# Kernel tuning notes

Measured on AMD Instinct MI355X. Metric: run time of the kernel, lower is better.

The kernel has to match this reference:

```python
import jax, jax.numpy as jnp
import numpy as np

D_MODEL = 1024
N_HEAD = 16
D_HEAD = D_MODEL // N_HEAD
B, S = 4, 2048


def setup_inputs() -> dict:
    key = jax.random.key(0)
    ks = jax.random.split(key, 9)
    s = 1.0 / np.sqrt(D_MODEL)
    inp = {"x": jax.random.normal(ks[0], (B, S, D_MODEL), dtype=jnp.float32)}
    for i, name in enumerate(["q", "k", "v", "o"]):
        inp[f"W{name}"] = jax.random.uniform(ks[1 + 2 * i], (D_MODEL, D_MODEL), jnp.float32, -s, s)
        inp[f"b{name}"] = jax.random.uniform(ks[2 + 2 * i], (D_MODEL,), jnp.float32, -s, s)
    return inp


def reference(x, Wq, bq, Wk, bk, Wv, bv, Wo, bo):
    b, sq, _ = x.shape
    skv = sq
    # projections (torch Linear: x @ W^T + b), reshape to (b, h, s, d)
    def proj(W, bias):
        return (x @ W.T + bias).reshape(b, sq, N_HEAD, D_HEAD).transpose(0, 2, 1, 3)
    q, k, v = proj(Wq, bq), proj(Wk, bk), proj(Wv, bv)
    scale = np.sqrt(D_HEAD).astype(np.float32)
    scores = jnp.einsum("bhqd,bhkd->bhqk", q, k) / scale
    causal_mask = jnp.triu(jnp.ones((sq, skv), dtype=bool), k=1)
    scores = jnp.where(causal_mask, -jnp.inf, scores)
    attn = jax.nn.softmax(scores, axis=-1)
    o = jnp.einsum("bhqk,bhkd->bhqd", attn, v)  # (b, h, sq, d_head)
    o = o.transpose(0, 2, 1, 3).reshape(b, sq, D_MODEL)
    return o @ Wo.T + bo
```

## Files before the change

### kernel.cpp

```cpp
#include <hip/hip_runtime.h>
#include <hip/hip_bf16.h>
#include <math.h>

#define S_LEN 2048
#define DMODEL 1024
#define NHEAD 16
#define DHEAD 64
#define BATCH 4
#define MROWS (BATCH * S_LEN)

typedef unsigned short u16;
typedef __attribute__((ext_vector_type(4))) unsigned short u16x4;
typedef __attribute__((ext_vector_type(2))) unsigned u32x2;
typedef __attribute__((ext_vector_type(8))) short bf16x8;
typedef __attribute__((ext_vector_type(4))) float f32x4;

#define GLDS16(g, l)                                              \
  __builtin_amdgcn_global_load_lds(                               \
      (const __attribute__((address_space(1))) void*)(g),         \
      (__attribute__((address_space(3))) void*)(l), 16, 0, 0)

__device__ __forceinline__ u16 f2bf(float f) {
  unsigned u = __float_as_uint(f);
  u += 0x7fff + ((u >> 16) & 1);
  return (u16)(u >> 16);
}

__device__ __forceinline__ float exp2v(float x) {
  float r;
  asm("v_exp_f32 %0, %1" : "=v"(r) : "v"(x));
  return r;
}

__device__ __forceinline__ f32x4 mfma16(bf16x8 a, bf16x8 b, f32x4 c) {
  return __builtin_amdgcn_mfma_f32_16x16x32_bf16(a, b, c, 0, 0, 0);
}

__global__ __launch_bounds__(256) void castk(const float* __restrict__ in,
                                             u16* __restrict__ out, int n) {
  int i = (blockIdx.x * 256 + threadIdx.x) * 4;
  if (i >= n) return;
  f32x4 v = *(const f32x4*)(in + i);
  u16 a0 = f2bf(v[0]), a1 = f2bf(v[1]), a2 = f2bf(v[2]), a3 = f2bf(v[3]);
  out[i + 0] = a0; out[i + 1] = a1; out[i + 2] = a2; out[i + 3] = a3;
}

__global__ __launch_bounds__(256) void castw(
    const float* __restrict__ i0, const float* __restrict__ i1,
    const float* __restrict__ i2, const float* __restrict__ i3,
    u16* __restrict__ o0, u16* __restrict__ o1,
    u16* __restrict__ o2, u16* __restrict__ o3) {
  const int m = blockIdx.y;
  const float* in = m == 0 ? i0 : (m == 1 ? i1 : (m == 2 ? i2 : i3));
  u16* out = m == 0 ? o0 : (m == 1 ? o1 : (m == 2 ? o2 : o3));
  int i = (blockIdx.x * 256 + threadIdx.x) * 4;
  f32x4 v = *(const f32x4*)(in + i);
  u16 a0 = f2bf(v[0]), a1 = f2bf(v[1]), a2 = f2bf(v[2]), a3 = f2bf(v[3]);
  out[i + 0] = a0; out[i + 1] = a1; out[i + 2] = a2; out[i + 3] = a3;
}

__global__ __launch_bounds__(256) void gemm_qkv(
    const u16* __restrict__ Xb,
    const u16* __restrict__ W0, const u16* __restrict__ W1, const u16* __restrict__ W2,
    const float* __restrict__ b0, const float* __restrict__ b1, const float* __restrict__ b2,
    u16* __restrict__ O0, u16* __restrict__ O1, u16* __restrict__ O2) {
  __shared__ u16 As[128 * 64];
  __shared__ u16 Bs[128 * 64];
  const int flat = blockIdx.x;
  const int xcd = flat & 7, idx = flat >> 3;
  const int ymt = xcd * 8 + idx / 24;
  const int rem = idx % 24;
  const int xnt = rem & 7;
  const int z = rem >> 3;
  const u16* Wm = z == 0 ? W0 : (z == 1 ? W1 : W2);
  const float* bias = z == 0 ? b0 : (z == 1 ? b1 : b2);
  u16* Out = z == 0 ? O0 : (z == 1 ? O1 : O2);
  const float qs = (z == 0) ? 0.18033688011112042f : 1.0f;
  const int tid = threadIdx.x;
  const int wave = tid >> 6, lane = tid & 63, g = lane >> 4, c = lane & 15;
  const int wm = wave >> 1, wn = wave & 1;
  const int bm0 = ymt * 128, bn0 = xnt * 128;

  f32x4 acc[4][4];
#pragma unroll
  for (int m = 0; m < 4; ++m)
#pragma unroll
    for (int n = 0; n < 4; ++n) acc[m][n] = (f32x4){0.f, 0.f, 0.f, 0.f};

  for (int k0 = 0; k0 < DMODEL; k0 += 64) {
    __syncthreads();
#pragma unroll
    for (int cc = 0; cc < 4; ++cc) {
      const int ci = cc * 256 + tid;
      const int row = ci >> 3, ch = ci & 7;
      const int sc = ((ch ^ (row & 7)) << 3);
      GLDS16(Xb + (size_t)(bm0 + row) * DMODEL + k0 + sc,
             (char*)As + (cc * 256 + wave * 64) * 16);
      GLDS16(Wm + (size_t)(bn0 + row) * DMODEL + k0 + sc,
             (char*)Bs + (cc * 256 + wave * 64) * 16);
    }
    __syncthreads();
#pragma unroll
    for (int ks = 0; ks < 2; ++ks) {
      bf16x8 af[4], bfr[4];
#pragma unroll
      for (int m = 0; m < 4; ++m) {
        const int arow = wm * 64 + m * 16 + c;
        af[m] = *(const bf16x8*)((const char*)As + arow * 128 +
                                 (((ks * 4 + g) ^ (arow & 7)) << 4));
      }
#pragma unroll
      for (int n = 0; n < 4; ++n) {
        const int brow = wn * 64 + n * 16 + c;
        bfr[n] = *(const bf16x8*)((const char*)Bs + brow * 128 +
                                  (((ks * 4 + g) ^ (brow & 7)) << 4));
      }
#pragma unroll
      for (int m = 0; m < 4; ++m)
#pragma unroll
        for (int n = 0; n < 4; ++n)
          acc[m][n] = mfma16(af[m], bfr[n], acc[m][n]);
    }
  }
  if (z < 2) {
#pragma unroll
    for (int n = 0; n < 4; ++n) {
      const int coln = bn0 + wn * 64 + n * 16 + c;
      const float bn_ = bias[coln];
      const int h = coln >> 6, d = coln & 63;
#pragma unroll
      for (int m = 0; m < 4; ++m) {
#pragma unroll
        for (int r = 0; r < 4; ++r) {
          const int rowm = bm0 + wm * 64 + m * 16 + g * 4 + r;
          const int b_ = rowm >> 11, s_ = rowm & 2047;
          Out[(((size_t)(b_ * NHEAD + h) * S_LEN + s_) << 6) + d] =
              f2bf((acc[m][n][r] + bn_) * qs);
        }
      }
    }
  } else {
#pragma unroll
    for (int n = 0; n < 4; ++n) {
      const int coln = bn0 + wn * 64 + n * 16 + c;
      const float bn_ = bias[coln];
      const int h = coln >> 6, d = coln & 63;
#pragma unroll
      for (int m = 0; m < 4; ++m) {
        const int row0 = bm0 + wm * 64 + m * 16 + g * 4;
        const int b_ = row0 >> 11, s_ = row0 & 2047;
        u16x4 pk;
#pragma unroll
        for (int r = 0; r < 4; ++r) pk[r] = f2bf(acc[m][n][r] + bn_);
        *(u16x4*)(Out + ((size_t)(b_ * NHEAD + h) * DHEAD + d) * S_LEN + s_) = pk;
      }
    }
  }
}

__global__ __launch_bounds__(256) void gemm_out(
    const u16* __restrict__ Ab, const u16* __restrict__ Wm,
    const float* __restrict__ bias, float* __restrict__ Out) {
  __shared__ u16 As[128 * 64];
  __shared__ u16 Bs[128 * 64];
  const int flat = blockIdx.x;
  const int xcd = flat & 7, idx = flat >> 3;
  const int ymt = xcd * 8 + (idx >> 3);
  const int xnt = idx & 7;
  const int tid = threadIdx.x;
  const int wave = tid >> 6, lane = tid & 63, g = lane >> 4, c = lane & 15;
  const int wm = wave >> 1, wn = wave & 1;
  const int bm0 = ymt * 128, bn0 = xnt * 128;

  f32x4 acc[4][4];
#pragma unroll
  for (int m = 0; m < 4; ++m)
#pragma unroll
    for (int n = 0; n < 4; ++n) acc[m][n] = (f32x4){0.f, 0.f, 0.f, 0.f};

  for (int k0 = 0; k0 < DMODEL; k0 += 64) {
    __syncthreads();
#pragma unroll
    for (int cc = 0; cc < 4; ++cc) {
      const int ci = cc * 256 + tid;
      const int row = ci >> 3, ch = ci & 7;
      const int sc = ((ch ^ (row & 7)) << 3);
      GLDS16(Ab + (size_t)(bm0 + row) * DMODEL + k0 + sc,
             (char*)As + (cc * 256 + wave * 64) * 16);
      GLDS16(Wm + (size_t)(bn0 + row) * DMODEL + k0 + sc,
             (char*)Bs + (cc * 256 + wave * 64) * 16);
    }
    __syncthreads();
#pragma unroll
    for (int ks = 0; ks < 2; ++ks) {
      bf16x8 af[4], bfr[4];
#pragma unroll
      for (int m = 0; m < 4; ++m) {
        const int arow = wm * 64 + m * 16 + c;
        af[m] = *(const bf16x8*)((const char*)As + arow * 128 +
                                 (((ks * 4 + g) ^ (arow & 7)) << 4));
      }
#pragma unroll
      for (int n = 0; n < 4; ++n) {
        const int brow = wn * 64 + n * 16 + c;
        bfr[n] = *(const bf16x8*)((const char*)Bs + brow * 128 +
                                  (((ks * 4 + g) ^ (brow & 7)) << 4));
      }
#pragma unroll
      for (int m = 0; m < 4; ++m)
#pragma unroll
        for (int n = 0; n < 4; ++n)
          acc[m][n] = mfma16(af[m], bfr[n], acc[m][n]);
    }
  }
#pragma unroll
  for (int n = 0; n < 4; ++n) {
    const int coln = bn0 + wn * 64 + n * 16 + c;
    const float bn_ = bias[coln];
#pragma unroll
    for (int m = 0; m < 4; ++m) {
#pragma unroll
      for (int r = 0; r < 4; ++r) {
        const int rowm = bm0 + wm * 64 + m * 16 + g * 4 + r;
        Out[(size_t)rowm * DMODEL + coln] = acc[m][n][r] + bn_;
      }
    }
  }
}

__global__ __launch_bounds__(256) void attn_fwd(const u16* __restrict__ Qb,
                                                const u16* __restrict__ Kb,
                                                const u16* __restrict__ VTb,
                                                u16* __restrict__ AOb) {
  __shared__ u16 Kt[2][64 * 64];
  __shared__ u16 Vt[2][64 * 64];
  const int tid = threadIdx.x;
  const int w = tid >> 6, lane = tid & 63, g = lane >> 4, c = lane & 15;
  const int ghi = g >> 1;
  const int srcA = ((g & 1) << 5) + c;
  const int srcB = srcA + 16;
  const int flat = blockIdx.x;
  const int wg = (flat & 7) * 128 + (flat >> 3);
  const int bh = wg >> 4;
  const int pr = wg & 15;
  const size_t base = (size_t)bh * (S_LEN * DHEAD);
  const int b_ = bh >> 4, h = bh & 15;
  const int ci0 = w * 64 + lane;

#define STAGE(buf_, kt_) do {                                              \
    const int kv0_ = (kt_) * 64;                                           \
    _Pragma("unroll")                                                      \
    for (int call = 0; call < 2; ++call) {                                 \
      const int ci = call * 256 + ci0;                                     \
      const int row_ = ci >> 3;                                            \
      const int colg = (ci & 7) ^ (row_ & 7);                              \
      GLDS16(Kb + base + (size_t)(kv0_ + row_) * 64 + colg * 8,            \
             (char*)Kt[buf_] + (call * 256 + w * 64) * 16);                \
      GLDS16(VTb + base + (size_t)row_ * S_LEN + kv0_ + colg * 8,          \
             (char*)Vt[buf_] + (call * 256 + w * 64) * 16);                \
    }                                                                      \
  } while (0)

#pragma unroll
  for (int pass = 0; pass < 2; ++pass) {
    const int qt = pass ? pr : (31 - pr);
    const int qb = qt * 64;
    const int q = qb + w * 16 + c;
    const bf16x8 qf0 = *(const bf16x8*)(Qb + base + (size_t)q * 64 + g * 8);
    const bf16x8 qf1 = *(const bf16x8*)(Qb + base + (size_t)q * 64 + 32 + g * 8);

    f32x4 oacc[4];
#pragma unroll
    for (int dt = 0; dt < 4; ++dt) oacc[dt] = (f32x4){0.f, 0.f, 0.f, 0.f};
    float m = -30000.f, l = 0.f;

    const int nt = qt + 1;
    STAGE(0, 0);
    for (int kt = 0; kt < nt; ++kt) {
      const int kv0 = kt * 64;
      const int cur = kt & 1;
      if (kt + 1 < nt) {
        STAGE((kt + 1) & 1, kt + 1);
        asm volatile("s_waitcnt vmcnt(4)" ::: "memory");
      } else {
        asm volatile("s_waitcnt vmcnt(0)" ::: "memory");
      }
      __builtin_amdgcn_s_barrier();

      f32x4 s[4];
#pragma unroll
      for (int t = 0; t < 4; ++t) {
        const int krow = t * 16 + c;
        const char* kbase = (const char*)Kt[cur] + krow * 128;
        bf16x8 kf0 = *(const bf16x8*)(kbase + ((g ^ (krow & 7)) * 16));
        bf16x8 kf1 = *(const bf16x8*)(kbase + (((4 + g) ^ (krow & 7)) * 16));
        f32x4 zacc = (f32x4){0.f, 0.f, 0.f, 0.f};
        zacc = mfma16(kf0, qf0, zacc);
        zacc = mfma16(kf1, qf1, zacc);
        s[t] = zacc;
      }
      if (kt == nt - 1) {
#pragma unroll
        for (int t = 0; t < 4; ++t)
#pragma unroll
          for (int r = 0; r < 4; ++r)
            if (kv0 + t * 16 + 4 * g + r > q) s[t][r] = -30000.f;
      }
      const float a0 = fmaxf(fmaxf(s[0][0], s[0][1]), s[0][2]);
      const float a1 = fmaxf(fmaxf(s[0][3], s[1][0]), s[1][1]);
      const float a2 = fmaxf(fmaxf(s[1][2], s[1][3]), s[2][0]);
      const float a3 = fmaxf(fmaxf(s[2][1], s[2][2]), s[2][3]);
      const float a4 = fmaxf(fmaxf(s[3][0], s[3][1]), s[3][2]);
      float pm = fmaxf(fmaxf(fmaxf(a0, a1), a2), fmaxf(fmaxf(a3, a4), s[3][3]));
      pm = fmaxf(pm, __shfl_xor(pm, 16));
      pm = fmaxf(pm, __shfl_xor(pm, 32));
      if (__any(pm > m + 8.0f)) {
        const float mn = fmaxf(m, pm);
        const float sc = exp2v(m - mn);
        l *= sc;
#pragma unroll
        for (int dt = 0; dt < 4; ++dt) oacc[dt] *= sc;
        m = mn;
      }
      float rs = 0.f;
      unsigned pk[4][2];
#pragma unroll
      for (int t = 0; t < 4; ++t) {
        const float p0 = exp2v(s[t][0] - m), p1 = exp2v(s[t][1] - m);
        const float p2 = exp2v(s[t][2] - m), p3 = exp2v(s[t][3] - m);
        rs += (p0 + p1) + (p2 + p3);
        const unsigned q0 = __float_as_uint(p0) + 0x8000u;
        const unsigned q1 = __float_as_uint(p1) + 0x8000u;
        const unsigned q2 = __float_as_uint(p2) + 0x8000u;
        const unsigned q3 = __float_as_uint(p3) + 0x8000u;
        pk[t][0] = __builtin_amdgcn_perm(q1, q0, 0x07060302u);
        pk[t][1] = __builtin_amdgcn_perm(q3, q2, 0x07060302u);
      }
      rs += __shfl_xor(rs, 16);
      rs += __shfl_xor(rs, 32);
      l += rs;

#pragma unroll
      for (int kk = 0; kk < 2; ++kk) {
        union { int u[4]; bf16x8 v; } pb;
#pragma unroll
        for (int hh = 0; hh < 2; ++hh) {
          const int eA = __shfl((int)pk[2 * kk][hh], srcA);
          const int oA = __shfl((int)pk[2 * kk + 1][hh], srcA);
          const int eB = __shfl((int)pk[2 * kk][hh], srcB);
          const int oB = __shfl((int)pk[2 * kk + 1][hh], srcB);
          pb.u[hh] = ghi ? oA : eA;
          pb.u[2 + hh] = ghi ? oB : eB;
        }
#pragma unroll
        for (int dt = 0; dt < 4; ++dt) {
          const int vrow = dt * 16 + c;
          const bf16x8 vf = *(const bf16x8*)((const char*)Vt[cur] + vrow * 128 +
                                             (((kk * 4 + g) ^ (vrow & 7)) * 16));
          oacc[dt] = mfma16(vf, pb.v, oacc[dt]);
        }
      }
      __builtin_amdgcn_s_barrier();
    }
    const float inv = 1.0f / l;
    const size_t rowbase = ((size_t)(b_ * S_LEN + q) * DMODEL) + h * 64;
#pragma unroll
    for (int dt = 0; dt < 4; ++dt) {
      u16x4 pk4;
#pragma unroll
      for (int r = 0; r < 4; ++r) pk4[r] = f2bf(oacc[dt][r] * inv);
      *(u16x4*)(AOb + rowbase + dt * 16 + 4 * g) = pk4;
    }
  }
#undef STAGE
}

extern "C" void kernel_launch(void* const* d_in, const int* in_sizes, int n_in,
                              void* d_out, int out_size, void* d_ws, size_t ws_size,
                              hipStream_t stream) {
  const float* x  = (const float*)d_in[0];
  const float* Wq = (const float*)d_in[1];
  const float* bq = (const float*)d_in[2];
  const float* Wk = (const float*)d_in[3];
  const float* bk = (const float*)d_in[4];
  const float* Wv = (const float*)d_in[5];
  const float* bv = (const float*)d_in[6];
  const float* Wo = (const float*)d_in[7];
  const float* bo = (const float*)d_in[8];
  float* out = (float*)d_out;
  char* ws = (char*)d_ws;

  const size_t MB = 1024 * 1024;
  u16* xb  = (u16*)(ws);
  u16* Wqb = (u16*)(ws + 16 * MB);
  u16* Wkb = (u16*)(ws + 18 * MB);
  u16* Wvb = (u16*)(ws + 20 * MB);
  u16* Wob = (u16*)(ws + 22 * MB);
  u16* Qb  = (u16*)(ws + 24 * MB);
  u16* Kb  = (u16*)(ws + 40 * MB);
  u16* VTb = (u16*)(ws + 56 * MB);
  u16* AOb = (u16*)(ws + 72 * MB);

  castk<<<8192, 256, 0, stream>>>(x, xb, MROWS * DMODEL);
  castw<<<dim3(1024, 4), 256, 0, stream>>>(Wq, Wk, Wv, Wo, Wqb, Wkb, Wvb, Wob);

  gemm_qkv<<<1536, 256, 0, stream>>>(
      xb, Wqb, Wkb, Wvb, bq, bk, bv, Qb, Kb, VTb);

  attn_fwd<<<1024, 256, 0, stream>>>(Qb, Kb, VTb, AOb);

  gemm_out<<<512, 256, 0, stream>>>(AOb, Wob, bo, out);
}
```

Before: 188.0 us.

## Use 128-key single-buffered KV tiles in causal attention kernel

The attention loop now processes 128 keys per iteration instead of 64, so it runs half as many iterations with fewer barriers and fewer softmax max/rescale steps per key. The double-buffered async prefetch of the next K/V tile is removed; each tile is loaded synchronously into one larger shared buffer between two __syncthreads. The V swizzle is widened to 16 chunks to match the new row width. The cost is that load latency is no longer overlapped with MFMA work, and when the causal diagonal falls in the first half of a tile, the extra 64 masked keys are still computed.

```diff
diff --git a/kernel.cpp b/kernel.cpp
--- a/kernel.cpp
+++ b/kernel.cpp
@@ -11,7 +11,6 @@
 
 typedef unsigned short u16;
 typedef __attribute__((ext_vector_type(4))) unsigned short u16x4;
-typedef __attribute__((ext_vector_type(2))) unsigned u32x2;
 typedef __attribute__((ext_vector_type(8))) short bf16x8;
 typedef __attribute__((ext_vector_type(4))) float f32x4;
 
@@ -232,8 +231,8 @@
                                                 const u16* __restrict__ Kb,
                                                 const u16* __restrict__ VTb,
                                                 u16* __restrict__ AOb) {
-  __shared__ u16 Kt[2][64 * 64];
-  __shared__ u16 Vt[2][64 * 64];
+  __shared__ u16 Kt[128 * 64];
+  __shared__ u16 Vt[64 * 128];
   const int tid = threadIdx.x;
   const int w = tid >> 6, lane = tid & 63, g = lane >> 4, c = lane & 15;
   const int ghi = g >> 1;
@@ -245,21 +244,6 @@
   const int pr = wg & 15;
   const size_t base = (size_t)bh * (S_LEN * DHEAD);
   const int b_ = bh >> 4, h = bh & 15;
-  const int ci0 = w * 64 + lane;
-
-#define STAGE(buf_, kt_) do {                                              \
-    const int kv0_ = (kt_) * 64;                                           \
-    _Pragma("unroll")                                                      \
-    for (int call = 0; call < 2; ++call) {                                 \
-      const int ci = call * 256 + ci0;                                     \
-      const int row_ = ci >> 3;                                            \
-      const int colg = (ci & 7) ^ (row_ & 7);                              \
-      GLDS16(Kb + base + (size_t)(kv0_ + row_) * 64 + colg * 8,            \
-             (char*)Kt[buf_] + (call * 256 + w * 64) * 16);                \
-      GLDS16(VTb + base + (size_t)row_ * S_LEN + kv0_ + colg * 8,          \
-             (char*)Vt[buf_] + (call * 256 + w * 64) * 16);                \
-    }                                                                      \
-  } while (0)
 
 #pragma unroll
   for (int pass = 0; pass < 2; ++pass) {
@@ -274,26 +258,29 @@
     for (int dt = 0; dt < 4; ++dt) oacc[dt] = (f32x4){0.f, 0.f, 0.f, 0.f};
     float m = -30000.f, l = 0.f;
 
-    const int nt = qt + 1;
-    STAGE(0, 0);
+    const int nt = (qt + 2) >> 1;
     for (int kt = 0; kt < nt; ++kt) {
-      const int kv0 = kt * 64;
-      const int cur = kt & 1;
-      if (kt + 1 < nt) {
-        STAGE((kt + 1) & 1, kt + 1);
-        asm volatile("s_waitcnt vmcnt(4)" ::: "memory");
-      } else {
-        asm volatile("s_waitcnt vmcnt(0)" ::: "memory");
-      }
-      __builtin_amdgcn_s_barrier();
-
-      f32x4 s[4];
-#pragma unroll
-      for (int t = 0; t < 4; ++t) {
+      const int kv0 = kt * 128;
+      __syncthreads();
+#pragma unroll
+      for (int cc = 0; cc < 4; ++cc) {
+        const int ci = cc * 256 + tid;
+        const int krow = ci >> 3, kch = ci & 7;
+        GLDS16(Kb + base + (size_t)(kv0 + krow) * 64 + ((kch ^ (krow & 7)) << 3),
+               (char*)Kt + (cc * 256 + w * 64) * 16);
+        const int vrow = ci >> 4, vch = ci & 15;
+        GLDS16(VTb + base + (size_t)vrow * S_LEN + kv0 + ((vch ^ (vrow & 15)) << 3),
+               (char*)Vt + (cc * 256 + w * 64) * 16);
+      }
+      __syncthreads();
+
+      f32x4 s[8];
+#pragma unroll
+      for (int t = 0; t < 8; ++t) {
         const int krow = t * 16 + c;
-        const char* kbase = (const char*)Kt[cur] + krow * 128;
-        bf16x8 kf0 = *(const bf16x8*)(kbase + ((g ^ (krow & 7)) * 16));
-        bf16x8 kf1 = *(const bf16x8*)(kbase + (((4 + g) ^ (krow & 7)) * 16));
+        const char* kbase = (const char*)Kt + krow * 128;
+        bf16x8 kf0 = *(const bf16x8*)(kbase + ((g ^ (krow & 7)) << 4));
+        bf16x8 kf1 = *(const bf16x8*)(kbase + (((4 + g) ^ (krow & 7)) << 4));
         f32x4 zacc = (f32x4){0.f, 0.f, 0.f, 0.f};
         zacc = mfma16(kf0, qf0, zacc);
         zacc = mfma16(kf1, qf1, zacc);
@@ -301,17 +288,16 @@
       }
       if (kt == nt - 1) {
 #pragma unroll
-        for (int t = 0; t < 4; ++t)
+        for (int t = 0; t < 8; ++t)
 #pragma unroll
           for (int r = 0; r < 4; ++r)
             if (kv0 + t * 16 + 4 * g + r > q) s[t][r] = -30000.f;
       }
-      const float a0 = fmaxf(fmaxf(s[0][0], s[0][1]), s[0][2]);
-      const float a1 = fmaxf(fmaxf(s[0][3], s[1][0]), s[1][1]);
-      const float a2 = fmaxf(fmaxf(s[1][2], s[1][3]), s[2][0]);
-      const float a3 = fmaxf(fmaxf(s[2][1], s[2][2]), s[2][3]);
-      const float a4 = fmaxf(fmaxf(s[3][0], s[3][1]), s[3][2]);
-      float pm = fmaxf(fmaxf(fmaxf(a0, a1), a2), fmaxf(fmaxf(a3, a4), s[3][3]));
+      float pm = s[0][0];
+#pragma unroll
+      for (int t = 0; t < 8; ++t)
+#pragma unroll
+        for (int r = 0; r < 4; ++r) pm = fmaxf(pm, s[t][r]);
       pm = fmaxf(pm, __shfl_xor(pm, 16));
       pm = fmaxf(pm, __shfl_xor(pm, 32));
       if (__any(pm > m + 8.0f)) {
@@ -323,9 +309,9 @@
         m = mn;
       }
       float rs = 0.f;
-      unsigned pk[4][2];
-#pragma unroll
-      for (int t = 0; t < 4; ++t) {
+      unsigned pk[8][2];
+#pragma unroll
+      for (int t = 0; t < 8; ++t) {
         const float p0 = exp2v(s[t][0] - m), p1 = exp2v(s[t][1] - m);
         const float p2 = exp2v(s[t][2] - m), p3 = exp2v(s[t][3] - m);
         rs += (p0 + p1) + (p2 + p3);
@@ -341,7 +327,7 @@
       l += rs;
 
 #pragma unroll
-      for (int kk = 0; kk < 2; ++kk) {
+      for (int kk = 0; kk < 4; ++kk) {
         union { int u[4]; bf16x8 v; } pb;
 #pragma unroll
         for (int hh = 0; hh < 2; ++hh) {
@@ -355,12 +341,11 @@
 #pragma unroll
         for (int dt = 0; dt < 4; ++dt) {
           const int vrow = dt * 16 + c;
-          const bf16x8 vf = *(const bf16x8*)((const char*)Vt[cur] + vrow * 128 +
-                                             (((kk * 4 + g) ^ (vrow & 7)) * 16));
+          const bf16x8 vf = *(const bf16x8*)((const char*)Vt + vrow * 256 +
+                                             (((kk * 4 + g) ^ (vrow & 15)) << 4));
           oacc[dt] = mfma16(vf, pb.v, oacc[dt]);
         }
       }
-      __builtin_amdgcn_s_barrier();
     }
     const float inv = 1.0f / l;
     const size_t rowbase = ((size_t)(b_ * S_LEN + q) * DMODEL) + h * 64;
@@ -372,7 +357,6 @@
       *(u16x4*)(AOb + rowbase + dt * 16 + 4 * g) = pk4;
     }
   }
-#undef STAGE
 }
 
 extern "C" void kernel_launch(void* const* d_in, const int* in_sizes, int n_in,
```

Measured after the change: 196.4 us. 1.04x slower.
